# Optimization experiments

Measured on AMD Instinct MI355X. Metric: run time of the kernel, lower is better.

## Reference

```python
import jax, jax.numpy as jnp
import numpy as np

N_NODES = 50000
N_EDGES = 800000
IN_C, OUT_C, EDGE_F, HEADS, HID, FINAL = 8, 16, 8, 4, 64, 128
NEG_SLOPE = 0.2  # PyG GATConv default LeakyReLU slope


def setup_inputs() -> dict:
    key = jax.random.key(0)
    ks = jax.random.split(key, 12)
    s = 0.1
    return {
        "x": jax.random.normal(ks[0], (N_NODES, IN_C), jnp.float32),
        "edge_index": jax.random.randint(ks[1], (2, N_EDGES), 0, N_NODES, jnp.int64),
        "edge_attr": jax.random.normal(ks[2], (N_EDGES, EDGE_F), jnp.float32),
        # NNConv params: root weight, bias, edge-MLP Linear(EDGE_F -> IN_C*OUT_C)
        "ecc_root": jax.random.normal(ks[3], (IN_C, OUT_C), jnp.float32) * s,
        "ecc_bias": jnp.zeros((OUT_C,), jnp.float32),
        "mlp_w": jax.random.normal(ks[4], (EDGE_F, IN_C * OUT_C), jnp.float32) * s,
        "mlp_b": jnp.zeros((IN_C * OUT_C,), jnp.float32),
        # GATConv params
        "gat_lin": jax.random.normal(ks[5], (OUT_C, HEADS * HID), jnp.float32) * s,
        "att_src": jax.random.normal(ks[6], (HEADS, HID), jnp.float32) * s,
        "att_dst": jax.random.normal(ks[7], (HEADS, HID), jnp.float32) * s,
        "gat_bias": jnp.zeros((HEADS * HID,), jnp.float32),
        # final Linear
        "fc_w": jax.random.normal(ks[8], (HEADS * HID, FINAL), jnp.float32) * s,
        "fc_b": jnp.zeros((FINAL,), jnp.float32),
    }


def _forward(x, edge_index, edge_attr, ecc_root, ecc_bias, mlp_w, mlp_b,
             gat_lin, att_src, att_dst, gat_bias, fc_w, fc_b):
    src, dst = edge_index[0], edge_index[1]  # messages flow src -> dst

    # ---- NNConv (edge-conditioned conv), aggr='add' ----
    # per-edge weight matrices [E, IN_C, OUT_C] from edge MLP
    w_e = (edge_attr @ mlp_w + mlp_b).reshape(-1, IN_C, OUT_C)
    msg = jnp.einsum('ei,eio->eo', x[src], w_e)                 # [E, OUT_C]
    agg = jax.ops.segment_sum(msg, dst, num_segments=N_NODES)   # [N, OUT_C]
    h = jax.nn.relu(x @ ecc_root + agg + ecc_bias)              # [N, OUT_C]

    # ---- GATConv (heads concatenated) ----
    g = (h @ gat_lin).reshape(N_NODES, HEADS, HID)              # [N, H, D]
    a_src = jnp.einsum('nhd,hd->nh', g, att_src)                # [N, H]
    a_dst = jnp.einsum('nhd,hd->nh', g, att_dst)
    e = jax.nn.leaky_relu(a_src[src] + a_dst[dst], NEG_SLOPE)   # [E, H]
    # segment softmax over incoming edges of each dst node
    e_max = jax.ops.segment_max(e, dst, num_segments=N_NODES)   # [N, H]
    e_max = jnp.where(jnp.isfinite(e_max), e_max, 0.0)
    e_exp = jnp.exp(e - e_max[dst])                             # [E, H]
    denom = jax.ops.segment_sum(e_exp, dst, num_segments=N_NODES)
    alpha = e_exp / (denom[dst] + 1e-16)                        # [E, H]
    out = jax.ops.segment_sum(alpha[:, :, None] * g[src], dst,
                              num_segments=N_NODES)             # [N, H, D]
    out = jax.nn.relu(out.reshape(N_NODES, HEADS * HID) + gat_bias)

    # ---- final linear ----
    return out @ fc_w + fc_b                                    # [N, FINAL]


def reference(x, edge_index, edge_attr, ecc_root, ecc_bias, mlp_w, mlp_b,
              gat_lin, att_src, att_dst, gat_bias, fc_w, fc_b):
    return _forward(x, edge_index, edge_attr, ecc_root, ecc_bias, mlp_w, mlp_b,
                    gat_lin, att_src, att_dst, gat_bias, fc_w, fc_b)
```

## Files before the change

### kernel.cpp

```cpp
#include <hip/hip_runtime.h>

#define N_NODES 50000
#define N_EDGES 800000
#define IN_C 8
#define OUT_C 16
#define EDGE_F 8
#define HEADS 4
#define HID 64
#define GDIM (HEADS*HID)
#define FINAL 128
#define NEG_SLOPE 0.2f
#define EB ((N_EDGES+255)/256)
#define YB ((N_NODES*16+255)/256)
#define NBLK 196

__device__ __forceinline__ int clampn(int v) {
    return v < 0 ? 0 : (v >= N_NODES ? N_NODES - 1 : v);
}
__device__ __forceinline__ unsigned short f32_to_bf16(float f) {
    unsigned u = __float_as_uint(f);
    unsigned r = (u + 0x7fffu + ((u >> 16) & 1u)) >> 16;
    return (unsigned short)r;
}
__device__ __forceinline__ float bf16lo(unsigned u) { return __uint_as_float(u << 16); }
__device__ __forceinline__ float bf16hi(unsigned u) { return __uint_as_float(u & 0xffff0000u); }

__global__ __launch_bounds__(256) void k_hist(const int* __restrict__ dst,
                                              int* __restrict__ cnt,
                                              int* __restrict__ rnk)
{
    int e = blockIdx.x * 256 + threadIdx.x;
    if (e >= N_EDGES) return;
    rnk[e] = atomicAdd(&cnt[clampn(dst[e])], 1);
}

__global__ __launch_bounds__(256) void k_part(const int* __restrict__ cnt,
                                              int* __restrict__ part)
{
    int i = blockIdx.x * 256 + threadIdx.x;
    int v = (i < N_NODES) ? cnt[i] : 0;
#pragma unroll
    for (int off = 32; off; off >>= 1) v += __shfl_down(v, off);
    __shared__ int ws[4];
    if ((threadIdx.x & 63) == 0) ws[threadIdx.x >> 6] = v;
    __syncthreads();
    if (threadIdx.x == 0) part[blockIdx.x] = ws[0] + ws[1] + ws[2] + ws[3];
}

__global__ __launch_bounds__(256) void k_scan1(const int* __restrict__ part,
                                               int* __restrict__ partscan)
{
    int t = threadIdx.x;
    int v = (t < NBLK) ? part[t] : 0;
    int lane = t & 63, wid = t >> 6;
    int incl = v;
#pragma unroll
    for (int off = 1; off < 64; off <<= 1) {
        int u = __shfl_up(incl, off);
        if (lane >= off) incl += u;
    }
    __shared__ int wsum[4];
    if (lane == 63) wsum[wid] = incl;
    __syncthreads();
    int add = 0;
    for (int w = 0; w < wid; w++) add += wsum[w];
    partscan[t] = incl - v + add;
}

__global__ __launch_bounds__(256) void k_add(const int* __restrict__ cnt,
                                             const int* __restrict__ partscan,
                                             int* __restrict__ offs)
{
    int i = blockIdx.x * 256 + threadIdx.x;
    int v = (i < N_NODES) ? cnt[i] : 0;
    int lane = threadIdx.x & 63, wid = threadIdx.x >> 6;
    int incl = v;
#pragma unroll
    for (int off = 1; off < 64; off <<= 1) {
        int u = __shfl_up(incl, off);
        if (lane >= off) incl += u;
    }
    __shared__ int wsum[4];
    if (lane == 63) wsum[wid] = incl;
    __syncthreads();
    int add = partscan[blockIdx.x];
    for (int w = 0; w < wid; w++) add += wsum[w];
    if (i < N_NODES) offs[i] = incl - v + add;
    if (i == 0) offs[N_NODES] = N_EDGES;
}

__global__ __launch_bounds__(256) void k_scatter(
    const int* __restrict__ src, const int* __restrict__ dst,
    const int* __restrict__ rnk, const int* __restrict__ offs,
    int2* __restrict__ se_csr)
{
    int e = blockIdx.x * 256 + threadIdx.x;
    if (e >= N_EDGES) return;
    int p = offs[clampn(dst[e])] + rnk[e];
    se_csr[p] = make_int2(clampn(src[e]), e);
}

__global__ __launch_bounds__(256) void k0_y(
    const float* __restrict__ x, const float* __restrict__ mlp_w,
    uint4* __restrict__ Y4)
{
    __shared__ float smw[EDGE_F * IN_C * OUT_C];
    for (int i = threadIdx.x; i < EDGE_F * IN_C * OUT_C; i += 256) smw[i] = mlp_w[i];
    __syncthreads();

    int t = blockIdx.x * 256 + threadIdx.x;
    int n = t >> 4, o = t & 15;
    if (n >= N_NODES) return;

    float xv[IN_C];
#pragma unroll
    for (int i = 0; i < IN_C; i++) xv[i] = x[n * IN_C + i];

    unsigned pk[4];
#pragma unroll
    for (int f2 = 0; f2 < EDGE_F; f2 += 2) {
        float y0 = 0.f, y1 = 0.f;
#pragma unroll
        for (int i = 0; i < IN_C; i++) {
            y0 += xv[i] * smw[f2 * (IN_C * OUT_C) + i * OUT_C + o];
            y1 += xv[i] * smw[(f2 + 1) * (IN_C * OUT_C) + i * OUT_C + o];
        }
        pk[f2 >> 1] = (unsigned)f32_to_bf16(y0) | ((unsigned)f32_to_bf16(y1) << 16);
    }
    Y4[(size_t)n * OUT_C + o] = make_uint4(pk[0], pk[1], pk[2], pk[3]);
}

__global__ __launch_bounds__(256) void k2c_node(
    const float* __restrict__ x, const uint4* __restrict__ Y4,
    const int2* __restrict__ se_csr, const int* __restrict__ offs,
    const float* __restrict__ ea, const float* __restrict__ mlp_b,
    const float* __restrict__ ecc_root, const float* __restrict__ ecc_bias,
    const float* __restrict__ gat_lin,
    const float* __restrict__ att_src_w, const float* __restrict__ att_dst_w,
    unsigned short* __restrict__ g_bf, float* __restrict__ asrc, float* __restrict__ adst)
{
    int wid = threadIdx.x >> 6, lane = threadIdx.x & 63;
    int n = blockIdx.x * 4 + wid;
    if (n >= N_NODES) return;

    int o = lane & 15, el = lane >> 4;
    int beg = offs[n], end = offs[n + 1];

    float aggv = 0.f, xs = 0.f;
    for (int j = beg + el; j < end; j += 4) {
        int2 se = se_csr[j];
        int s = se.x, e = se.y;
        float4 a0 = *(const float4*)&ea[(size_t)e * EDGE_F];
        float4 a1 = *(const float4*)&ea[(size_t)e * EDGE_F + 4];
        uint4 yv = Y4[(size_t)s * OUT_C + o];
        aggv += a0.x * bf16lo(yv.x) + a0.y * bf16hi(yv.x)
              + a0.z * bf16lo(yv.y) + a0.w * bf16hi(yv.y)
              + a1.x * bf16lo(yv.z) + a1.y * bf16hi(yv.z)
              + a1.z * bf16lo(yv.w) + a1.w * bf16hi(yv.w);
        xs += x[s * IN_C + (o & 7)];
    }
    aggv += __shfl_down(aggv, 32);
    aggv += __shfl_down(aggv, 16);
    xs += __shfl_down(xs, 32);
    xs += __shfl_down(xs, 16);

    float hv = 0.f;
    if (lane < 16) {
        float v = ecc_bias[o] + aggv;
#pragma unroll
        for (int i = 0; i < IN_C; i++) {
            float xsi = __shfl(xs, i);
            v += xsi * mlp_b[i * OUT_C + o];
            v += x[n * IN_C + i] * ecc_root[i * OUT_C + o];
        }
        hv = fmaxf(v, 0.f);
    }

    float gv[4] = {0.f, 0.f, 0.f, 0.f};
#pragma unroll
    for (int k = 0; k < OUT_C; k++) {
        float hk = __shfl(hv, k);
#pragma unroll
        for (int j = 0; j < 4; j++)
            gv[j] += hk * gat_lin[k * GDIM + j * 64 + lane];
    }
#pragma unroll
    for (int j = 0; j < 4; j++)
        g_bf[(size_t)n * GDIM + j * 64 + lane] = f32_to_bf16(gv[j]);

    float vs[4], vd[4];
#pragma unroll
    for (int j = 0; j < 4; j++) {
        vs[j] = gv[j] * att_src_w[j * 64 + lane];
        vd[j] = gv[j] * att_dst_w[j * 64 + lane];
    }
#pragma unroll
    for (int off = 32; off; off >>= 1) {
#pragma unroll
        for (int j = 0; j < 4; j++) {
            vs[j] += __shfl_down(vs[j], off);
            vd[j] += __shfl_down(vd[j], off);
        }
    }
    if (lane == 0) {
#pragma unroll
        for (int j = 0; j < 4; j++) {
            asrc[n * HEADS + j] = vs[j];
            adst[n * HEADS + j] = vd[j];
        }
    }
}

__global__ __launch_bounds__(256) void k_gat(
    const int* __restrict__ offs, const int2* __restrict__ se_csr,
    const float* __restrict__ asrc, const float* __restrict__ adst,
    const unsigned short* __restrict__ g_bf, unsigned short* __restrict__ outg)
{
    int n = blockIdx.x, t = threadIdx.x;
    int lane32 = t & 31, grp = t >> 5;
    int hh = lane32 >> 3;
    int beg = offs[n], deg = offs[n + 1] - beg;

    float adsth = adst[n * HEADS + hh];

    float acc[8];
#pragma unroll
    for (int k = 0; k < 8; k++) acc[k] = 0.f;
    float denp = 0.f;

    for (int j = grp; j < deg; j += 8) {
        int s = se_csr[beg + j].x;
        float v = asrc[s * HEADS + hh] + adsth;
        v = v > 0.f ? v : NEG_SLOPE * v;
        float p = __expf(v);
        denp += p;
        uint4 gv = *(const uint4*)&g_bf[(size_t)s * GDIM + lane32 * 8];
        acc[0] += p * bf16lo(gv.x);
        acc[1] += p * bf16hi(gv.x);
        acc[2] += p * bf16lo(gv.y);
        acc[3] += p * bf16hi(gv.y);
        acc[4] += p * bf16lo(gv.z);
        acc[5] += p * bf16hi(gv.z);
        acc[6] += p * bf16lo(gv.w);
        acc[7] += p * bf16hi(gv.w);
    }

    __shared__ float s_acc[8][GDIM];
    __shared__ float s_den[8][HEADS];
    *(float4*)&s_acc[grp][lane32 * 8]     = make_float4(acc[0], acc[1], acc[2], acc[3]);
    *(float4*)&s_acc[grp][lane32 * 8 + 4] = make_float4(acc[4], acc[5], acc[6], acc[7]);
    if ((lane32 & 7) == 0) s_den[grp][hh] = denp;
    __syncthreads();

    int head = t >> 6;
    float den = 0.f, v = 0.f;
#pragma unroll
    for (int g2 = 0; g2 < 8; g2++) {
        den += s_den[g2][head];
        v += s_acc[g2][t];
    }
    outg[(size_t)n * GDIM + t] = f32_to_bf16(v / (den + 1e-16f));
}

#define BM 64
#define BK6 16
__global__ __launch_bounds__(256) void k6_final(
    const unsigned short* __restrict__ outg, const float* __restrict__ gat_bias,
    const float* __restrict__ fc_w, const float* __restrict__ fc_b,
    float* __restrict__ y)
{
    __shared__ float sA[BK6][BM + 4];
    __shared__ float sW[BK6][FINAL];
    int tid = threadIdx.x;
    int r0 = blockIdx.x * BM;
    int tcol = (tid & 31) * 4;
    int trow = (tid >> 5) * 8;

    float acc[8][4];
#pragma unroll
    for (int r = 0; r < 8; r++)
#pragma unroll
        for (int c = 0; c < 4; c++) acc[r][c] = 0.f;

    int ar = tid >> 2;
    int ak = (tid & 3) * 4;

    for (int k0 = 0; k0 < GDIM; k0 += BK6) {
        int row = r0 + ar;
        float4 av = make_float4(0.f, 0.f, 0.f, 0.f);
        if (row < N_NODES) {
            uint2 raw = *(const uint2*)&outg[(size_t)row * GDIM + k0 + ak];
            av = make_float4(bf16lo(raw.x), bf16hi(raw.x), bf16lo(raw.y), bf16hi(raw.y));
        }
        float4 bv = *(const float4*)&gat_bias[k0 + ak];
        av.x = fmaxf(av.x + bv.x, 0.f);
        av.y = fmaxf(av.y + bv.y, 0.f);
        av.z = fmaxf(av.z + bv.z, 0.f);
        av.w = fmaxf(av.w + bv.w, 0.f);
        sA[ak + 0][ar] = av.x;
        sA[ak + 1][ar] = av.y;
        sA[ak + 2][ar] = av.z;
        sA[ak + 3][ar] = av.w;
#pragma unroll
        for (int p = 0; p < 2; p++) {
            int kk = (tid >> 5) + p * 8;
            int c = (tid & 31) * 4;
            *(float4*)&sW[kk][c] = *(const float4*)&fc_w[(size_t)(k0 + kk) * FINAL + c];
        }
        __syncthreads();
#pragma unroll
        for (int kk = 0; kk < BK6; kk++) {
            float4 w = *(const float4*)&sW[kk][tcol];
            float4 a0 = *(const float4*)&sA[kk][trow];
            float4 a1 = *(const float4*)&sA[kk][trow + 4];
            float a[8] = {a0.x, a0.y, a0.z, a0.w, a1.x, a1.y, a1.z, a1.w};
#pragma unroll
            for (int r = 0; r < 8; r++) {
                acc[r][0] += a[r] * w.x;
                acc[r][1] += a[r] * w.y;
                acc[r][2] += a[r] * w.z;
                acc[r][3] += a[r] * w.w;
            }
        }
        __syncthreads();
    }

    float4 fb = *(const float4*)&fc_b[tcol];
#pragma unroll
    for (int r = 0; r < 8; r++) {
        int row = r0 + trow + r;
        if (row < N_NODES) {
            *(float4*)&y[(size_t)row * FINAL + tcol] =
                make_float4(acc[r][0] + fb.x, acc[r][1] + fb.y,
                            acc[r][2] + fb.z, acc[r][3] + fb.w);
        }
    }
}

extern "C" void kernel_launch(void* const* d_in, const int* in_sizes, int n_in,
                              void* d_out, int out_size, void* d_ws, size_t ws_size,
                              hipStream_t stream)
{
    const float* x        = (const float*)d_in[0];
    const int*   ei       = (const int*)d_in[1];
    const float* ea       = (const float*)d_in[2];
    const float* ecc_root = (const float*)d_in[3];
    const float* ecc_bias = (const float*)d_in[4];
    const float* mlp_w    = (const float*)d_in[5];
    const float* mlp_b    = (const float*)d_in[6];
    const float* gat_lin  = (const float*)d_in[7];
    const float* att_src  = (const float*)d_in[8];
    const float* att_dst  = (const float*)d_in[9];
    const float* gat_bias = (const float*)d_in[10];
    const float* fc_w     = (const float*)d_in[11];
    const float* fc_b     = (const float*)d_in[12];
    float* y = (float*)d_out;

    const int* src = ei;
    const int* dst = ei + N_EDGES;

    uint4* Y4 = (uint4*)d_ws;
    unsigned short* g_bf = (unsigned short*)(Y4 + (size_t)N_NODES * OUT_C);
    unsigned short* outg = g_bf + (size_t)N_NODES * GDIM;
    float* asrc = (float*)(outg + (size_t)N_NODES * GDIM);
    float* adst = asrc + (size_t)N_NODES * HEADS;
    int*   cnt      = (int*)(adst + (size_t)N_NODES * HEADS);
    int*   offs     = cnt + N_NODES;
    int*   part     = offs + N_NODES + 1;
    int*   partscan = part + 256;
    int*   rnk      = partscan + 256;
    int2*  se_csr   = (int2*)(rnk + N_EDGES);

    hipMemsetAsync(cnt, 0, sizeof(int) * N_NODES, stream);

    k_hist   <<<EB, 256, 0, stream>>>(dst, cnt, rnk);
    k0_y     <<<YB, 256, 0, stream>>>(x, mlp_w, Y4);
    k_part   <<<NBLK, 256, 0, stream>>>(cnt, part);
    k_scan1  <<<1, 256, 0, stream>>>(part, partscan);
    k_add    <<<NBLK, 256, 0, stream>>>(cnt, partscan, offs);
    k_scatter<<<EB, 256, 0, stream>>>(src, dst, rnk, offs, se_csr);

    k2c_node <<<(N_NODES + 3) / 4, 256, 0, stream>>>(x, Y4, se_csr, offs, ea, mlp_b,
                                                     ecc_root, ecc_bias, gat_lin,
                                                     att_src, att_dst, g_bf, asrc, adst);
    k_gat    <<<N_NODES, 256, 0, stream>>>(offs, se_csr, asrc, adst, g_bf, outg);
    k6_final <<<(N_NODES + BM - 1) / BM, 256, 0, stream>>>(outg, gat_bias, fc_w, fc_b, y);
}
```

Baseline: 375.9 us.

## Aggregate edge_attr⊗x outer products per node, then apply mlp_w once

Removes the k0_y precompute kernel that stored a bf16 Y table (x projected through mlp_w per node). Instead, each node's wave accumulates the 8x8 outer products of edge_attr and source x over its incoming edges and contracts that 64-vector with mlp_w held in shared memory. Gathers per edge drop from a 64-byte Y row plus edge_attr to one float of edge_attr and one float of x per lane, and the fp32 path avoids bf16 rounding of Y. In exchange each block loads mlp_w into shared memory and adds a __syncthreads, and the 16 lanes that compute h run a 64-step shared-memory dot product.

```diff
diff --git a/kernel.cpp b/kernel.cpp
--- a/kernel.cpp
+++ b/kernel.cpp
@@ -11,7 +11,6 @@
 #define FINAL 128
 #define NEG_SLOPE 0.2f
 #define EB ((N_EDGES+255)/256)
-#define YB ((N_NODES*16+255)/256)
 #define NBLK 196
 
 __device__ __forceinline__ int clampn(int v) {
@@ -100,78 +99,70 @@
     se_csr[p] = make_int2(clampn(src[e]), e);
 }
 
-__global__ __launch_bounds__(256) void k0_y(
-    const float* __restrict__ x, const float* __restrict__ mlp_w,
-    uint4* __restrict__ Y4)
-{
-    __shared__ float smw[EDGE_F * IN_C * OUT_C];
-    for (int i = threadIdx.x; i < EDGE_F * IN_C * OUT_C; i += 256) smw[i] = mlp_w[i];
-    __syncthreads();
-
-    int t = blockIdx.x * 256 + threadIdx.x;
-    int n = t >> 4, o = t & 15;
-    if (n >= N_NODES) return;
-
-    float xv[IN_C];
-#pragma unroll
-    for (int i = 0; i < IN_C; i++) xv[i] = x[n * IN_C + i];
-
-    unsigned pk[4];
-#pragma unroll
-    for (int f2 = 0; f2 < EDGE_F; f2 += 2) {
-        float y0 = 0.f, y1 = 0.f;
-#pragma unroll
-        for (int i = 0; i < IN_C; i++) {
-            y0 += xv[i] * smw[f2 * (IN_C * OUT_C) + i * OUT_C + o];
-            y1 += xv[i] * smw[(f2 + 1) * (IN_C * OUT_C) + i * OUT_C + o];
-        }
-        pk[f2 >> 1] = (unsigned)f32_to_bf16(y0) | ((unsigned)f32_to_bf16(y1) << 16);
-    }
-    Y4[(size_t)n * OUT_C + o] = make_uint4(pk[0], pk[1], pk[2], pk[3]);
-}
-
-__global__ __launch_bounds__(256) void k2c_node(
-    const float* __restrict__ x, const uint4* __restrict__ Y4,
+__global__ __launch_bounds__(256) void k2T_node(
+    const float* __restrict__ x,
     const int2* __restrict__ se_csr, const int* __restrict__ offs,
-    const float* __restrict__ ea, const float* __restrict__ mlp_b,
+    const float* __restrict__ ea,
+    const float* __restrict__ mlp_w, const float* __restrict__ mlp_b,
     const float* __restrict__ ecc_root, const float* __restrict__ ecc_bias,
     const float* __restrict__ gat_lin,
     const float* __restrict__ att_src_w, const float* __restrict__ att_dst_w,
     unsigned short* __restrict__ g_bf, float* __restrict__ asrc, float* __restrict__ adst)
 {
+    __shared__ float smW[EDGE_F * IN_C * OUT_C];
+    __shared__ float smb[IN_C * OUT_C];
+    __shared__ float sT[4][64];
+    __shared__ float sxs[4][8];
+    for (int i = threadIdx.x; i < EDGE_F * IN_C * OUT_C; i += 256) smW[i] = mlp_w[i];
+    for (int i = threadIdx.x; i < IN_C * OUT_C; i += 256) smb[i] = mlp_b[i];
+
     int wid = threadIdx.x >> 6, lane = threadIdx.x & 63;
     int n = blockIdx.x * 4 + wid;
-    if (n >= N_NODES) return;
-
-    int o = lane & 15, el = lane >> 4;
-    int beg = offs[n], end = offs[n + 1];
-
-    float aggv = 0.f, xs = 0.f;
-    for (int j = beg + el; j < end; j += 4) {
-        int2 se = se_csr[j];
-        int s = se.x, e = se.y;
-        float4 a0 = *(const float4*)&ea[(size_t)e * EDGE_F];
-        float4 a1 = *(const float4*)&ea[(size_t)e * EDGE_F + 4];
-        uint4 yv = Y4[(size_t)s * OUT_C + o];
-        aggv += a0.x * bf16lo(yv.x) + a0.y * bf16hi(yv.x)
-              + a0.z * bf16lo(yv.y) + a0.w * bf16hi(yv.y)
-              + a1.x * bf16lo(yv.z) + a1.y * bf16hi(yv.z)
-              + a1.z * bf16lo(yv.w) + a1.w * bf16hi(yv.w);
-        xs += x[s * IN_C + (o & 7)];
-    }
-    aggv += __shfl_down(aggv, 32);
-    aggv += __shfl_down(aggv, 16);
-    xs += __shfl_down(xs, 32);
-    xs += __shfl_down(xs, 16);
-
+    bool alive = (n < N_NODES);
+
+    float t0 = 0.f, t1 = 0.f, t2 = 0.f, t3 = 0.f, xs = 0.f;
+    if (alive) {
+        int f = lane >> 3, i = lane & 7;
+        int beg = offs[n], end = offs[n + 1];
+        int j = beg;
+        for (; j + 3 < end; j += 4) {
+            int2 se0 = se_csr[j],     se1 = se_csr[j + 1];
+            int2 se2 = se_csr[j + 2], se3 = se_csr[j + 3];
+            float a0 = ea[(size_t)se0.y * EDGE_F + f];
+            float a1 = ea[(size_t)se1.y * EDGE_F + f];
+            float a2 = ea[(size_t)se2.y * EDGE_F + f];
+            float a3 = ea[(size_t)se3.y * EDGE_F + f];
+            float x0 = x[se0.x * IN_C + i];
+            float x1 = x[se1.x * IN_C + i];
+            float x2 = x[se2.x * IN_C + i];
+            float x3 = x[se3.x * IN_C + i];
+            t0 += a0 * x0; t1 += a1 * x1; t2 += a2 * x2; t3 += a3 * x3;
+            xs += (x0 + x1) + (x2 + x3);
+        }
+        for (; j < end; j++) {
+            int2 se = se_csr[j];
+            float a = ea[(size_t)se.y * EDGE_F + f];
+            float xv = x[se.x * IN_C + i];
+            t0 += a * xv;
+            xs += xv;
+        }
+        sT[wid][lane] = (t0 + t1) + (t2 + t3);
+        if (f == 0) sxs[wid][i] = xs;
+    }
+    __syncthreads();
+    if (!alive) return;
+
+    int o = lane & 15;
     float hv = 0.f;
     if (lane < 16) {
-        float v = ecc_bias[o] + aggv;
-#pragma unroll
-        for (int i = 0; i < IN_C; i++) {
-            float xsi = __shfl(xs, i);
-            v += xsi * mlp_b[i * OUT_C + o];
-            v += x[n * IN_C + i] * ecc_root[i * OUT_C + o];
+        float v = ecc_bias[o];
+#pragma unroll 8
+        for (int jj = 0; jj < 64; jj++)
+            v += smW[jj * OUT_C + o] * sT[wid][jj];
+#pragma unroll
+        for (int ii = 0; ii < IN_C; ii++) {
+            v += smb[ii * OUT_C + o] * sxs[wid][ii];
+            v += x[n * IN_C + ii] * ecc_root[ii * OUT_C + o];
         }
         hv = fmaxf(v, 0.f);
     }
@@ -359,8 +350,7 @@
     const int* src = ei;
     const int* dst = ei + N_EDGES;
 
-    uint4* Y4 = (uint4*)d_ws;
-    unsigned short* g_bf = (unsigned short*)(Y4 + (size_t)N_NODES * OUT_C);
+    unsigned short* g_bf = (unsigned short*)d_ws;
     unsigned short* outg = g_bf + (size_t)N_NODES * GDIM;
     float* asrc = (float*)(outg + (size_t)N_NODES * GDIM);
     float* adst = asrc + (size_t)N_NODES * HEADS;
@@ -374,13 +364,13 @@
     hipMemsetAsync(cnt, 0, sizeof(int) * N_NODES, stream);
 
     k_hist   <<<EB, 256, 0, stream>>>(dst, cnt, rnk);
-    k0_y     <<<YB, 256, 0, stream>>>(x, mlp_w, Y4);
     k_part   <<<NBLK, 256, 0, stream>>>(cnt, part);
     k_scan1  <<<1, 256, 0, stream>>>(part, partscan);
     k_add    <<<NBLK, 256, 0, stream>>>(cnt, partscan, offs);
     k_scatter<<<EB, 256, 0, stream>>>(src, dst, rnk, offs, se_csr);
 
-    k2c_node <<<(N_NODES + 3) / 4, 256, 0, stream>>>(x, Y4, se_csr, offs, ea, mlp_b,
+    k2T_node <<<(N_NODES + 3) / 4, 256, 0, stream>>>(x, se_csr, offs, ea,
+                                                     mlp_w, mlp_b,
                                                      ecc_root, ecc_bias, gat_lin,
                                                      att_src, att_dst, g_bf, asrc, adst);
     k_gat    <<<N_NODES, 256, 0, stream>>>(offs, se_csr, asrc, adst, g_bf, outg);
```

After: 374.3 us. About the same (-0.4%).
